# Kernel tuning notes

Hardware: AMD Instinct MI355X
Metric: run time of the kernel (lower is better)

The kernel has to match this reference:

```python
import jax, jax.numpy as jnp
import numpy as np

D = 1024
H = 16
HD = D // H  # 64
BASE = 10000.0


def _rope_tables(seq_len, dtype=jnp.float32):
    # inv_freq over even dims, rotate-half convention: emb = cat(freqs, freqs)
    inv_freq = 1.0 / (BASE ** (jnp.arange(0, HD, 2, dtype=jnp.float32) / HD))
    t = jnp.arange(seq_len, dtype=jnp.float32)
    freqs = jnp.einsum('i,j->ij', t, inv_freq)          # [S, HD/2]
    emb = jnp.concatenate([freqs, freqs], axis=-1)       # [S, HD]
    return jnp.cos(emb).astype(dtype), jnp.sin(emb).astype(dtype)


def _rotate_half(x):
    x1, x2 = jnp.split(x, 2, axis=-1)
    return jnp.concatenate([-x2, x1], axis=-1)


def setup_inputs() -> dict:
    key = jax.random.key(0)
    ks = jax.random.split(key, 5)
    B, S = 2, 2048
    scale = 0.02
    return {
        'x': jax.random.normal(ks[0], (B, S, D), dtype=jnp.float32),
        'wq': jax.random.normal(ks[1], (D, D), dtype=jnp.float32) * scale,
        'wk': jax.random.normal(ks[2], (D, D), dtype=jnp.float32) * scale,
        'wv': jax.random.normal(ks[3], (D, D), dtype=jnp.float32) * scale,
        'wo': jax.random.normal(ks[4], (D, D), dtype=jnp.float32) * scale,
    }


def reference(x, wq, wk, wv, wo):
    B, S, _ = x.shape
    # QKV projections (torch Linear: x @ W^T), split into heads -> [B, H, S, HD]
    def proj(w):
        return jnp.einsum('bsd,ed->bse', x, w).reshape(B, S, H, HD).transpose(0, 2, 1, 3)
    q, k, v = proj(wq), proj(wk), proj(wv)

    # RoPE (rotate-half)
    cos, sin = _rope_tables(S, x.dtype)                  # [S, HD]
    cos = cos[None, None, :, :]
    sin = sin[None, None, :, :]
    q = q * cos + _rotate_half(q) * sin
    k = k * cos + _rotate_half(k) * sin

    # causal scaled-dot-product attention
    scores = jnp.einsum('bhqd,bhkd->bhqk', q, k) / jnp.sqrt(jnp.array(HD, x.dtype))
    causal = jnp.tril(jnp.ones((S, S), dtype=bool))
    scores = jnp.where(causal[None, None], scores, jnp.finfo(x.dtype).min)
    attn = jax.nn.softmax(scores, axis=-1)
    out = jnp.einsum('bhqk,bhkd->bhqd', attn, v)         # [B, H, S, HD]

    out = out.transpose(0, 2, 1, 3).reshape(B, S, D)
    return jnp.einsum('bsd,ed->bse', out, wo)
```

## Files before the change

kernel.cpp:

```cpp
#include <hip/hip_runtime.h>
#include <cstdint>
#include <cstddef>

typedef unsigned short u16;
typedef unsigned int u32;
typedef __bf16 bf16x8 __attribute__((ext_vector_type(8)));
typedef float f32x4 __attribute__((ext_vector_type(4)));
typedef u16 u16x8 __attribute__((ext_vector_type(8)));
typedef u16 u16x4 __attribute__((ext_vector_type(4)));

#define DD 1024
#define HH 16
#define HDIM 64
#define BB 2
#define SS 2048
#define MM (BB * SS)
#define NQT 32

__device__ __forceinline__ u16 cvt(float f) {
  __bf16 h = (__bf16)f;
  return __builtin_bit_cast(u16, h);
}
__device__ __forceinline__ f32x4 mfma16(bf16x8 a, bf16x8 b, f32x4 c) {
  return __builtin_amdgcn_mfma_f32_16x16x32_bf16(a, b, c, 0, 0, 0);
}
__device__ __forceinline__ bf16x8 ld_bf8(const u16* p) {
  return __builtin_bit_cast(bf16x8, *(const u16x8*)p);
}
__device__ __forceinline__ void async16(const void* g, void* l) {
  __builtin_amdgcn_global_load_lds(
      (__attribute__((address_space(1))) void*)(uintptr_t)g,
      (__attribute__((address_space(3))) void*)l, 16, 0, 0);
}

__global__ void cast_all(const float* __restrict__ x, const float* __restrict__ wq,
                         const float* __restrict__ wk, const float* __restrict__ wv,
                         const float* __restrict__ wo, u16* __restrict__ xb,
                         u16* __restrict__ wqb, u16* __restrict__ wkb,
                         u16* __restrict__ wvb, u16* __restrict__ wob) {
  int i = blockIdx.x * 256 + threadIdx.x;
  const float* src;
  u16* dst;
  int off;
  if (i < (1 << 20)) {
    src = x; dst = xb; off = i;
  } else {
    int j = i - (1 << 20);
    int w = j >> 18;
    off = j & ((1 << 18) - 1);
    src = (w == 0) ? wq : (w == 1) ? wk : (w == 2) ? wv : wo;
    dst = (w == 0) ? wqb : (w == 1) ? wkb : (w == 2) ? wvb : wob;
  }
  float4 v = ((const float4*)src)[off];
  u16x4 o;
  o[0] = cvt(v.x); o[1] = cvt(v.y); o[2] = cvt(v.z); o[3] = cvt(v.w);
  *(u16x4*)&dst[(size_t)off * 4] = o;
}

__global__ __launch_bounds__(256) void gemm_qkv(
    const u16* __restrict__ xb, const u16* __restrict__ wq,
    const u16* __restrict__ wk, const u16* __restrict__ wv,
    u16* __restrict__ Qo, u16* __restrict__ Ko, u16* __restrict__ Vto) {
  __shared__ __align__(16) u16 As[128 * 32];
  __shared__ __align__(16) u16 Bs[128 * 32];
  const int t = threadIdx.x;
  const int w = t >> 6, l = t & 63, lane16 = l & 15, quad = l >> 4;
  const int m0 = blockIdx.x * 128, n0 = blockIdx.y * 128;
  const u16* wsel = (blockIdx.z == 0) ? wq : (blockIdx.z == 1) ? wk : wv;
  const int m_w = (w >> 1) * 64, n_w = (w & 1) * 64;
  const int srow = t >> 2, scol = (t & 3) * 8;

  f32x4 acc[4][4] = {};
  for (int kt = 0; kt < 32; ++kt) {
    const int k0 = kt * 32;
    async16(&xb[(size_t)(m0 + srow) * DD + k0 + scol], &As[t * 8]);
    async16(&xb[(size_t)(m0 + 64 + srow) * DD + k0 + scol], &As[2048 + t * 8]);
    async16(&wsel[(size_t)(n0 + srow) * DD + k0 + scol], &Bs[t * 8]);
    async16(&wsel[(size_t)(n0 + 64 + srow) * DD + k0 + scol], &Bs[2048 + t * 8]);
    __syncthreads();
    bf16x8 af[4], bfr[4];
#pragma unroll
    for (int mi = 0; mi < 4; ++mi)
      af[mi] = ld_bf8(&As[(m_w + mi * 16 + lane16) * 32 + quad * 8]);
#pragma unroll
    for (int ni = 0; ni < 4; ++ni)
      bfr[ni] = ld_bf8(&Bs[(n_w + ni * 16 + lane16) * 32 + quad * 8]);
#pragma unroll
    for (int mi = 0; mi < 4; ++mi)
#pragma unroll
      for (int ni = 0; ni < 4; ++ni)
        acc[mi][ni] = mfma16(af[mi], bfr[ni], acc[mi][ni]);
    __syncthreads();
  }
  if (blockIdx.z == 2) {
#pragma unroll
    for (int mi = 0; mi < 4; ++mi) {
      int mbase = m0 + m_w + mi * 16 + quad * 4;
      int b = mbase >> 11, s0 = mbase & (SS - 1);
#pragma unroll
      for (int ni = 0; ni < 4; ++ni) {
        int e = n0 + n_w + ni * 16 + lane16;
        int h = e >> 6, d = e & 63;
        u16x4 pk;
#pragma unroll
        for (int r = 0; r < 4; ++r) pk[r] = cvt(acc[mi][ni][r]);
        *(u16x4*)&Vto[((size_t)(b * HH + h) * HDIM + d) * SS + s0] = pk;
      }
    }
  } else {
    u16* osel = (blockIdx.z == 0) ? Qo : Ko;
    const float scale = (blockIdx.z == 0) ? 0.18033688f : 1.0f;
    float invf[2];
    invf[0] = exp2f((float)lane16 * -0.4152410119f) * 0.15915494309f;
    invf[1] = exp2f((float)(16 + lane16) * -0.4152410119f) * 0.15915494309f;
    const int h = (n0 + n_w) >> 6;
#pragma unroll
    for (int mi = 0; mi < 4; ++mi) {
#pragma unroll
      for (int r = 0; r < 4; ++r) {
        int mrow = m0 + m_w + mi * 16 + quad * 4 + r;
        int b = mrow >> 11, s = mrow & (SS - 1);
        size_t rowbase = ((size_t)(b * HH + h) * SS + s) * HDIM;
#pragma unroll
        for (int ni = 0; ni < 2; ++ni) {
          float x1 = acc[mi][ni][r], x2 = acc[mi][ni + 2][r];
          float rv = (float)s * invf[ni];
          rv = rv - floorf(rv);
          float sn = __builtin_amdgcn_sinf(rv);
          float c  = __builtin_amdgcn_cosf(rv);
          int d = ni * 16 + lane16;
          osel[rowbase + d]      = cvt((x1 * c - x2 * sn) * scale);
          osel[rowbase + d + 32] = cvt((x2 * c + x1 * sn) * scale);
        }
      }
    }
  }
}

__global__ __launch_bounds__(256, 3) void attn_k(const u16* __restrict__ Qb,
                                                 const u16* __restrict__ Kb,
                                                 const u16* __restrict__ Vt,
                                                 u16* __restrict__ AO) {
  __shared__ __align__(16) u16 KsF[128 * 64];
  __shared__ __align__(16) u16 VtL[64 * 128];
  __shared__ __align__(16) u16 Ps[4][16 * 136];
  const int t = threadIdx.x;
  const int w = t >> 6, l = t & 63, lane16 = l & 15, quad = l >> 4;
  const int bh = blockIdx.x;
  const int jj = NQT - 1 - (int)blockIdx.y;
  const size_t base = (size_t)bh * SS * HDIM;
  const u16* Qp = Qb + base;
  const int b = bh >> 4, h = bh & 15;

  const int q0 = jj * 64;
  const int qrow = q0 + w * 16 + lane16;
  bf16x8 qf0 = ld_bf8(&Qp[(size_t)qrow * 64 + quad * 8]);
  bf16x8 qf1 = ld_bf8(&Qp[(size_t)qrow * 64 + 32 + quad * 8]);

  u16x8 onesu;
#pragma unroll
  for (int i = 0; i < 8; ++i) onesu[i] = 0x3F80;
  const bf16x8 ones = __builtin_bit_cast(bf16x8, onesu);

  f32x4 o[4] = {};
  f32x4 lacc = {};

  const u16* kptr[4];
  const u16* vptr[4];
#pragma unroll
  for (int i = 0; i < 4; ++i) {
    int p = i * 256 + t;
    int r = p >> 3;
    int c = (p & 7) ^ (r & 7);
    kptr[i] = Kb + base + (size_t)r * 64 + c * 8;
    int d = p >> 4;
    int q = (p & 15) ^ (d & 15);
    vptr[i] = Vt + base + (size_t)d * SS + q * 8;
  }

  const int ktmax = jj >> 1;
  for (int kt = 0; kt <= ktmax; ++kt) {
    const int kv0 = kt * 128;
#pragma unroll
    for (int i = 0; i < 4; ++i) {
      async16(kptr[i], &KsF[(i * 256 + t) * 8]);
      kptr[i] += 128 * 64;
    }
#pragma unroll
    for (int i = 0; i < 4; ++i) {
      async16(vptr[i], &VtL[(i * 256 + t) * 8]);
      vptr[i] += 128;
    }
    __syncthreads();
    f32x4 sc[8];
#pragma unroll
    for (int nc = 0; nc < 8; ++nc) {
      int rr = nc * 16 + lane16;
      int p0 = rr * 8 + (quad ^ (rr & 7));
      int p1 = rr * 8 + ((4 + quad) ^ (rr & 7));
      f32x4 a = {0.f, 0.f, 0.f, 0.f};
      a = mfma16(qf0, ld_bf8(&KsF[p0 * 8]), a);
      a = mfma16(qf1, ld_bf8(&KsF[p1 * 8]), a);
      sc[nc] = a;
    }
    if (kt == ktmax) {
#pragma unroll
      for (int nc = 0; nc < 8; ++nc) {
        int col = kv0 + nc * 16 + lane16;
#pragma unroll
        for (int r = 0; r < 4; ++r) {
          int row = q0 + w * 16 + quad * 4 + r;
          if (col > row) sc[nc][r] = -3.0e38f;
        }
      }
    }
#pragma unroll
    for (int nc = 0; nc < 8; ++nc)
#pragma unroll
      for (int r = 0; r < 4; ++r) sc[nc][r] = exp2f(sc[nc][r]);
#pragma unroll
    for (int r = 0; r < 4; ++r)
#pragma unroll
      for (int nc = 0; nc < 8; ++nc)
        Ps[w][(quad * 4 + r) * 136 + nc * 16 + lane16] = cvt(sc[nc][r]);
    bf16x8 pf[4];
#pragma unroll
    for (int c = 0; c < 4; ++c)
      pf[c] = ld_bf8(&Ps[w][lane16 * 136 + c * 32 + quad * 8]);
#pragma unroll
    for (int nd = 0; nd < 4; ++nd) {
      int d = nd * 16 + lane16;
#pragma unroll
      for (int c = 0; c < 4; ++c) {
        bf16x8 bv = ld_bf8(&VtL[(size_t)d * 128 + (((c * 4 + quad) ^ lane16) * 8)]);
        o[nd] = mfma16(pf[c], bv, o[nd]);
      }
    }
#pragma unroll
    for (int c = 0; c < 4; ++c) lacc = mfma16(pf[c], ones, lacc);
    __syncthreads();
  }
#pragma unroll
  for (int r = 0; r < 4; ++r) {
    int srow = q0 + w * 16 + quad * 4 + r;
    float inv = 1.0f / lacc[r];
#pragma unroll
    for (int nd = 0; nd < 4; ++nd)
      AO[(size_t)(b * SS + srow) * DD + h * HDIM + nd * 16 + lane16] = cvt(o[nd][r] * inv);
  }
}

__global__ __launch_bounds__(256) void gemm_out(const u16* __restrict__ A, const u16* __restrict__ W,
                                                float* __restrict__ out) {
  __shared__ __align__(16) u16 As[128 * 32];
  __shared__ __align__(16) u16 Bs[128 * 32];
  const int t = threadIdx.x;
  const int w = t >> 6, l = t & 63, lane16 = l & 15, quad = l >> 4;
  const int m0 = blockIdx.x * 128, n0 = blockIdx.y * 128;
  const int m_w = (w >> 1) * 64, n_w = (w & 1) * 64;
  const int srow = t >> 2, scol = (t & 3) * 8;

  f32x4 acc[4][4] = {};
  for (int kt = 0; kt < 32; ++kt) {
    const int k0 = kt * 32;
    async16(&A[(size_t)(m0 + srow) * DD + k0 + scol], &As[t * 8]);
    async16(&A[(size_t)(m0 + 64 + srow) * DD + k0 + scol], &As[2048 + t * 8]);
    async16(&W[(size_t)(n0 + srow) * DD + k0 + scol], &Bs[t * 8]);
    async16(&W[(size_t)(n0 + 64 + srow) * DD + k0 + scol], &Bs[2048 + t * 8]);
    __syncthreads();
    bf16x8 af[4], bfr[4];
#pragma unroll
    for (int mi = 0; mi < 4; ++mi)
      af[mi] = ld_bf8(&As[(m_w + mi * 16 + lane16) * 32 + quad * 8]);
#pragma unroll
    for (int ni = 0; ni < 4; ++ni)
      bfr[ni] = ld_bf8(&Bs[(n_w + ni * 16 + lane16) * 32 + quad * 8]);
#pragma unroll
    for (int mi = 0; mi < 4; ++mi)
#pragma unroll
      for (int ni = 0; ni < 4; ++ni)
        acc[mi][ni] = mfma16(af[mi], bfr[ni], acc[mi][ni]);
    __syncthreads();
  }
#pragma unroll
  for (int mi = 0; mi < 4; ++mi) {
#pragma unroll
    for (int r = 0; r < 4; ++r) {
      int mrow = m0 + m_w + mi * 16 + quad * 4 + r;
#pragma unroll
      for (int ni = 0; ni < 4; ++ni) {
        int e = n0 + n_w + ni * 16 + lane16;
        out[(size_t)mrow * DD + e] = acc[mi][ni][r];
      }
    }
  }
}

extern "C" void kernel_launch(void* const* d_in, const int* in_sizes, int n_in,
                              void* d_out, int out_size, void* d_ws, size_t ws_size,
                              hipStream_t stream) {
  const float* x  = (const float*)d_in[0];
  const float* wq = (const float*)d_in[1];
  const float* wk = (const float*)d_in[2];
  const float* wv = (const float*)d_in[3];
  const float* wo = (const float*)d_in[4];
  float* out = (float*)d_out;
  char* ws = (char*)d_ws;

  u16* xb  = (u16*)(ws + (size_t)0);
  u16* wqb = (u16*)(ws + ((size_t)8  << 20));
  u16* wkb = (u16*)(ws + ((size_t)10 << 20));
  u16* wvb = (u16*)(ws + ((size_t)12 << 20));
  u16* wob = (u16*)(ws + ((size_t)14 << 20));
  u16* Qb  = (u16*)(ws + ((size_t)16 << 20));
  u16* Kb  = (u16*)(ws + ((size_t)24 << 20));
  u16* Vtg = (u16*)(ws + ((size_t)32 << 20));
  u16* AO  = (u16*)(ws + ((size_t)40 << 20));

  cast_all<<<8192, 256, 0, stream>>>(x, wq, wk, wv, wo, xb, wqb, wkb, wvb, wob);
  gemm_qkv<<<dim3(32, 8, 3), 256, 0, stream>>>(xb, wqb, wkb, wvb, Qb, Kb, Vtg);
  attn_k<<<dim3(32, 32), 256, 0, stream>>>(Qb, Kb, Vtg, AO);
  gemm_out<<<dim3(32, 8), 256, 0, stream>>>(AO, wob, out);
}
```

Baseline: 177.8 us.

## Transpose attention MFMA operands to compute S^T and shrink per-wave P staging

The attention kernel swaps the MFMA operand order so each lane holds scores for one query row across four consecutive keys. This lets P be written to LDS as packed 4-element vectors into a smaller XOR-swizzled 16x64 buffer processed in two halves, and lets the output be stored as packed vectors per row. Shrinking Ps reduces LDS use, and the launch-bounds occupancy hint is raised from 3 to 4 blocks. The cost is more register pressure under the higher occupancy target and a more intricate indexing scheme.

Measured after the change: 178.7 us. About the same (+0.5%).

```diff
diff --git a/kernel.cpp b/kernel.cpp
--- a/kernel.cpp
+++ b/kernel.cpp
@@ -137,13 +137,13 @@
   }
 }
 
-__global__ __launch_bounds__(256, 3) void attn_k(const u16* __restrict__ Qb,
+__global__ __launch_bounds__(256, 4) void attn_k(const u16* __restrict__ Qb,
                                                  const u16* __restrict__ Kb,
                                                  const u16* __restrict__ Vt,
                                                  u16* __restrict__ AO) {
   __shared__ __align__(16) u16 KsF[128 * 64];
   __shared__ __align__(16) u16 VtL[64 * 128];
-  __shared__ __align__(16) u16 Ps[4][16 * 136];
+  __shared__ __align__(16) u16 Ps[4][16 * 64];
   const int t = threadIdx.x;
   const int w = t >> 6, l = t & 63, lane16 = l & 15, quad = l >> 4;
   const int bh = blockIdx.x;
@@ -178,6 +178,7 @@
     vptr[i] = Vt + base + (size_t)d * SS + q * 8;
   }
 
+  u16* Pw = Ps[w];
   const int ktmax = jj >> 1;
   for (int kt = 0; kt <= ktmax; ++kt) {
     const int kv0 = kt * 128;
@@ -192,61 +193,65 @@
       vptr[i] += 128;
     }
     __syncthreads();
-    f32x4 sc[8];
+    f32x4 st[8];
 #pragma unroll
     for (int nc = 0; nc < 8; ++nc) {
       int rr = nc * 16 + lane16;
       int p0 = rr * 8 + (quad ^ (rr & 7));
       int p1 = rr * 8 + ((4 + quad) ^ (rr & 7));
       f32x4 a = {0.f, 0.f, 0.f, 0.f};
-      a = mfma16(qf0, ld_bf8(&KsF[p0 * 8]), a);
-      a = mfma16(qf1, ld_bf8(&KsF[p1 * 8]), a);
-      sc[nc] = a;
+      a = mfma16(ld_bf8(&KsF[p0 * 8]), qf0, a);
+      a = mfma16(ld_bf8(&KsF[p1 * 8]), qf1, a);
+      st[nc] = a;
     }
     if (kt == ktmax) {
 #pragma unroll
       for (int nc = 0; nc < 8; ++nc) {
-        int col = kv0 + nc * 16 + lane16;
-#pragma unroll
-        for (int r = 0; r < 4; ++r) {
-          int row = q0 + w * 16 + quad * 4 + r;
-          if (col > row) sc[nc][r] = -3.0e38f;
+        int kvb = kv0 + nc * 16 + quad * 4;
+#pragma unroll
+        for (int r = 0; r < 4; ++r)
+          if (kvb + r > qrow) st[nc][r] = -3.0e38f;
+      }
+    }
+#pragma unroll
+    for (int nc = 0; nc < 8; ++nc)
+#pragma unroll
+      for (int r = 0; r < 4; ++r) st[nc][r] = exp2f(st[nc][r]);
+#pragma unroll
+    for (int kh = 0; kh < 2; ++kh) {
+#pragma unroll
+      for (int ncr = 0; ncr < 4; ++ncr) {
+        f32x4 v = st[kh * 4 + ncr];
+        u16x4 pk;
+#pragma unroll
+        for (int r = 0; r < 4; ++r) pk[r] = cvt(v[r]);
+        int addr = lane16 * 64 + (((ncr * 2 + (quad >> 1)) ^ (lane16 & 7)) * 8) +
+                   (quad & 1) * 4;
+        *(u16x4*)&Pw[addr] = pk;
+      }
+#pragma unroll
+      for (int cf = 0; cf < 2; ++cf) {
+        bf16x8 pf = ld_bf8(&Pw[lane16 * 64 + (((cf * 4 + quad) ^ (lane16 & 7)) * 8)]);
+        lacc = mfma16(ones, pf, lacc);
+        int g = kh * 8 + cf * 4 + quad;
+#pragma unroll
+        for (int nd = 0; nd < 4; ++nd) {
+          int d = nd * 16 + lane16;
+          bf16x8 bv = ld_bf8(&VtL[(size_t)d * 128 + ((g ^ lane16) * 8)]);
+          o[nd] = mfma16(bv, pf, o[nd]);
         }
       }
     }
-#pragma unroll
-    for (int nc = 0; nc < 8; ++nc)
-#pragma unroll
-      for (int r = 0; r < 4; ++r) sc[nc][r] = exp2f(sc[nc][r]);
-#pragma unroll
-    for (int r = 0; r < 4; ++r)
-#pragma unroll
-      for (int nc = 0; nc < 8; ++nc)
-        Ps[w][(quad * 4 + r) * 136 + nc * 16 + lane16] = cvt(sc[nc][r]);
-    bf16x8 pf[4];
-#pragma unroll
-    for (int c = 0; c < 4; ++c)
-      pf[c] = ld_bf8(&Ps[w][lane16 * 136 + c * 32 + quad * 8]);
-#pragma unroll
-    for (int nd = 0; nd < 4; ++nd) {
-      int d = nd * 16 + lane16;
-#pragma unroll
-      for (int c = 0; c < 4; ++c) {
-        bf16x8 bv = ld_bf8(&VtL[(size_t)d * 128 + (((c * 4 + quad) ^ lane16) * 8)]);
-        o[nd] = mfma16(pf[c], bv, o[nd]);
-      }
-    }
-#pragma unroll
-    for (int c = 0; c < 4; ++c) lacc = mfma16(pf[c], ones, lacc);
-    __syncthreads();
-  }
-#pragma unroll
-  for (int r = 0; r < 4; ++r) {
-    int srow = q0 + w * 16 + quad * 4 + r;
-    float inv = 1.0f / lacc[r];
-#pragma unroll
-    for (int nd = 0; nd < 4; ++nd)
-      AO[(size_t)(b * SS + srow) * DD + h * HDIM + nd * 16 + lane16] = cvt(o[nd][r] * inv);
+    __syncthreads();
+  }
+  const float inv = 1.0f / lacc[0];
+  const size_t rowb = (size_t)(b * SS + qrow) * DD + h * HDIM + quad * 4;
+#pragma unroll
+  for (int nd = 0; nd < 4; ++nd) {
+    u16x4 pk;
+#pragma unroll
+    for (int r = 0; r < 4; ++r) pk[r] = cvt(o[nd][r] * inv);
+    *(u16x4*)&AO[rowb + nd * 16] = pk;
   }
 }
 
```
